# Kernel tuning notes

Hardware: AMD Instinct MI355X
Metric: run time of the kernel (lower is better)

Reference implementation:

```python
import jax, jax.numpy as jnp
import numpy as np

D_MODEL = 2048
NUM_HEADS = 16
KV_HEADS = 4
HEAD_DIM = D_MODEL // NUM_HEADS  # 128
SEQ = 4096
BATCH = 1
ROPE_THETA = 10000.0


def _rope_cache(T, dim, base, dtype):
    inv_freq = 1.0 / (base ** (jnp.arange(0, dim, 2, dtype=jnp.float32) / dim))
    t = jnp.arange(T, dtype=jnp.float32)
    freqs = jnp.outer(t, inv_freq)                      # (T, dim/2)
    emb = jnp.concatenate([freqs, freqs], axis=-1)      # (T, dim)
    return jnp.cos(emb).astype(dtype), jnp.sin(emb).astype(dtype)


def _rotate_half(x):
    d = x.shape[-1] // 2
    return jnp.concatenate([-x[..., d:], x[..., :d]], axis=-1)


def _apply_rope(q, k, cos, sin):
    # q: (B,T,Hq,D), k: (B,T,Hkv,D); cos/sin: (T,D) broadcast over heads
    c = cos[None, :, None, :]
    s = sin[None, :, None, :]
    q = q * c + _rotate_half(q) * s
    k = k * c + _rotate_half(k) * s
    return q, k


def setup_inputs() -> dict:
    key = jax.random.key(0)
    ks = jax.random.split(key, 6)
    sc = 1.0 / np.sqrt(D_MODEL)
    kv_out = KV_HEADS * HEAD_DIM
    return {
        "x": jax.random.normal(ks[0], (BATCH, SEQ, D_MODEL), dtype=jnp.float32),
        "Wq": jax.random.normal(ks[1], (D_MODEL, D_MODEL), dtype=jnp.float32) * sc,
        "Wk": jax.random.normal(ks[2], (D_MODEL, kv_out), dtype=jnp.float32) * sc,
        "Wv": jax.random.normal(ks[3], (D_MODEL, kv_out), dtype=jnp.float32) * sc,
        "Wo": jax.random.normal(ks[4], (D_MODEL, D_MODEL), dtype=jnp.float32) * sc,
        "bo": jax.random.normal(ks[5], (D_MODEL,), dtype=jnp.float32) * 0.01,
    }


def reference(x, Wq, Wk, Wv, Wo, bo):
    B, T, _ = x.shape
    q = (x @ Wq).reshape(B, T, NUM_HEADS, HEAD_DIM)
    k = (x @ Wk).reshape(B, T, KV_HEADS, HEAD_DIM)
    v = (x @ Wv).reshape(B, T, KV_HEADS, HEAD_DIM)

    cos, sin = _rope_cache(T, HEAD_DIM, ROPE_THETA, x.dtype)
    q, k = _apply_rope(q, k, cos, sin)

    reps = NUM_HEADS // KV_HEADS
    k = jnp.repeat(k, reps, axis=2)  # repeat_interleave on head dim
    v = jnp.repeat(v, reps, axis=2)

    # (B,H,T,D)
    q = q.transpose(0, 2, 1, 3)
    k = k.transpose(0, 2, 1, 3)
    v = v.transpose(0, 2, 1, 3)

    scores = jnp.einsum("bhqd,bhkd->bhqk", q, k)
    causal = jnp.triu(jnp.ones((T, T), dtype=bool), k=1)
    scores = jnp.where(causal[None, None], -jnp.inf, scores)
    attn = jax.nn.softmax(scores / jnp.sqrt(jnp.asarray(HEAD_DIM, x.dtype)), axis=-1)

    ctx = jnp.einsum("bhqk,bhkd->bhqd", attn, v)
    ctx = ctx.transpose(0, 2, 1, 3).reshape(B, T, D_MODEL)
    return ctx @ Wo + bo
```

## Files before the change

### kernel.cpp

```cpp
#include <hip/hip_runtime.h>
#include <cstdint>
#include <cstddef>

#define SEQ 4096
#define DM  2048
#define NH  16
#define KVH 4
#define HD  128
#define QSCALE (0.08838834764831845f * 1.4426950408889634f)

typedef short bf16_t;
typedef __attribute__((ext_vector_type(8))) short bf16x8;
typedef __attribute__((ext_vector_type(4))) float f32x4;
typedef __attribute__((ext_vector_type(4))) unsigned uint32x4;

__device__ __forceinline__ bf16_t f2b(float f) {
  unsigned u = __builtin_bit_cast(unsigned, f);
  u += 0x7fffu + ((u >> 16) & 1u);
  return (bf16_t)(u >> 16);
}
__device__ __forceinline__ float b2f(bf16_t s) {
  unsigned u = ((unsigned)(unsigned short)s) << 16;
  return __builtin_bit_cast(float, u);
}
__device__ __forceinline__ unsigned cvtpk(float lo, float hi) {
  unsigned r;
  asm("v_cvt_pk_bf16_f32 %0, %1, %2" : "=v"(r) : "v"(lo), "v"(hi));
  return r;
}

__device__ __forceinline__ void gload_lds16(const void* gsrc, void* ldst) {
  __builtin_amdgcn_global_load_lds(
      (__attribute__((address_space(1))) void*)gsrc,
      (__attribute__((address_space(3))) void*)ldst, 16, 0, 0);
}

__global__ void cast_x_bf16(const float* __restrict__ x, bf16_t* __restrict__ xb, int n4) {
  int i = blockIdx.x * 256 + threadIdx.x;
  if (i >= n4) return;
  float4 v = ((const float4*)x)[i];
  union { bf16_t h[4]; unsigned long long u; } o;
  o.h[0] = f2b(v.x); o.h[1] = f2b(v.y); o.h[2] = f2b(v.z); o.h[3] = f2b(v.w);
  ((unsigned long long*)xb)[i] = o.u;
}

__global__ void transpose_cast_w(const float* __restrict__ W, bf16_t* __restrict__ Wt,
                                 int K, int N) {
  __shared__ float tile[32][33];
  int k0 = blockIdx.y * 32, n0 = blockIdx.x * 32;
  int tx = threadIdx.x, ty = threadIdx.y;
#pragma unroll
  for (int dy = 0; dy < 32; dy += 8)
    tile[ty + dy][tx] = W[(size_t)(k0 + ty + dy) * N + n0 + tx];
  __syncthreads();
#pragma unroll
  for (int dy = 0; dy < 32; dy += 8)
    Wt[(size_t)(n0 + ty + dy) * K + k0 + tx] = f2b(tile[tx][ty + dy]);
}

__global__ void rope_tab(float* __restrict__ ct, float* __restrict__ st) {
  int i = blockIdx.x * 256 + threadIdx.x;
  if (i >= SEQ * 64) return;
  int t = i >> 6, j = i & 63;
  float invf = expf(-(float)j * (9.210340371976184f / 64.0f));
  float ang = (float)t * invf;
  ct[i] = cosf(ang);
  st[i] = sinf(ang);
}

__global__ void rope_apply(bf16_t* __restrict__ Qb, bf16_t* __restrict__ KVb,
                           const float* __restrict__ ct, const float* __restrict__ st) {
  int i = blockIdx.x * 256 + threadIdx.x;
  const int qtot = SEQ * NH * 64;
  const int tot = qtot + SEQ * KVH * 64;
  if (i >= tot) return;
  bf16_t* base; int t, j; float scl;
  if (i < qtot) {
    t = i >> 10; int rem = i & 1023; int hh = rem >> 6; j = rem & 63;
    base = Qb + (size_t)t * DM + hh * HD;
    scl = QSCALE;
  } else {
    int i2 = i - qtot;
    t = i2 >> 8; int rem = i2 & 255; int hh = rem >> 6; j = rem & 63;
    base = KVb + (size_t)t * 1024 + hh * HD;
    scl = 1.0f;
  }
  float c = ct[t * 64 + j], s = st[t * 64 + j];
  float x0 = b2f(base[j]);
  float x1 = b2f(base[j + 64]);
  base[j]      = f2b((x0 * c - x1 * s) * scl);
  base[j + 64] = f2b((x1 * c + x0 * s) * scl);
}

__global__ void transpose_v(const bf16_t* __restrict__ KVb, bf16_t* __restrict__ Vt) {
  __shared__ bf16_t tile[32][33];
  int t0 = blockIdx.y * 32, d0 = blockIdx.x * 32;
  int tx = threadIdx.x, ty = threadIdx.y;
#pragma unroll
  for (int dy = 0; dy < 32; dy += 8)
    tile[ty + dy][tx] = KVb[(size_t)(t0 + ty + dy) * 1024 + 512 + d0 + tx];
  __syncthreads();
  int tt = t0 + tx;
  int j = (tt & ~63) | (tt & 32) | ((tt & 12) << 1) | ((tt & 16) >> 2) | (tt & 3);
#pragma unroll
  for (int dy = 0; dy < 32; dy += 8)
    Vt[(size_t)(d0 + ty + dy) * SEQ + j] = tile[tx][ty + dy];
}

template <int BIAS>
__global__ __launch_bounds__(256, 2)
void gemm_bt(const bf16_t* __restrict__ A, const bf16_t* __restrict__ Bt,
             void* __restrict__ Cout, const float* __restrict__ bias,
             int M, int N, int K) {
  __shared__ __align__(16) bf16_t ldsA[128 * 64];
  __shared__ __align__(16) bf16_t ldsB[128 * 64];
  const int t = threadIdx.x;
  const int w = t >> 6, l = t & 63;
  const int lg = l >> 4, lr = l & 15;
  const int bm = blockIdx.y, bn = blockIdx.x;
  const int wr = (w >> 1) * 64, wc = (w & 1) * 64;

  f32x4 acc[4][4] = {};

  for (int k0 = 0; k0 < K; k0 += 64) {
    __syncthreads();
#pragma unroll
    for (int i = 0; i < 4; ++i) {
      int idx = i * 256 + t;
      int row = idx >> 3;
      int ch  = (idx & 7) ^ (row & 7);
      gload_lds16(A  + (size_t)(bm * 128 + row) * K + k0 + ch * 8, &ldsA[idx * 8]);
      gload_lds16(Bt + (size_t)(bn * 128 + row) * K + k0 + ch * 8, &ldsB[idx * 8]);
    }
    __syncthreads();
#pragma unroll
    for (int kk = 0; kk < 2; ++kk) {
      bf16x8 af[4], bfr[4];
#pragma unroll
      for (int m = 0; m < 4; ++m) {
        int row = wr + m * 16 + lr;
        int ch = (kk * 4 + lg) ^ (row & 7);
        af[m] = *(const bf16x8*)&ldsA[row * 64 + ch * 8];
      }
#pragma unroll
      for (int n = 0; n < 4; ++n) {
        int row = wc + n * 16 + lr;
        int ch = (kk * 4 + lg) ^ (row & 7);
        bfr[n] = *(const bf16x8*)&ldsB[row * 64 + ch * 8];
      }
#pragma unroll
      for (int m = 0; m < 4; ++m)
#pragma unroll
        for (int n = 0; n < 4; ++n)
          acc[m][n] = __builtin_amdgcn_mfma_f32_16x16x32_bf16(af[m], bfr[n], acc[m][n], 0, 0, 0);
    }
  }

  const int row0 = bm * 128 + wr + lg * 4;
  const int col0 = bn * 128 + wc + lr;
  if (BIAS) {
    float* C = (float*)Cout;
#pragma unroll
    for (int n = 0; n < 4; ++n) {
      int col = col0 + n * 16;
      float b = bias[col];
#pragma unroll
      for (int m = 0; m < 4; ++m)
#pragma unroll
        for (int r = 0; r < 4; ++r)
          C[(size_t)(row0 + m * 16 + r) * N + col] = acc[m][n][r] + b;
    }
  } else {
    bf16_t* C = (bf16_t*)Cout;
#pragma unroll
    for (int m = 0; m < 4; ++m)
#pragma unroll
      for (int n = 0; n < 4; ++n) {
        int col = col0 + n * 16;
#pragma unroll
        for (int r = 0; r < 4; ++r)
          C[(size_t)(row0 + m * 16 + r) * N + col] = f2b(acc[m][n][r]);
      }
  }
}

__global__ __launch_bounds__(256, 2)
void attn_fwd(const bf16_t* __restrict__ Qb, const bf16_t* __restrict__ KVb,
              const bf16_t* __restrict__ Vt, bf16_t* __restrict__ ctx) {
  __shared__ __align__(16) bf16_t kt[2][64 * 128];
  __shared__ __align__(16) bf16_t vts[2][128 * 64];

  const int t = threadIdx.x;
  const int w = t >> 6, l = t & 63;
  const int lg = l >> 4, lr = l & 15;
  const int h = blockIdx.y, g = h >> 2;
  const int b = blockIdx.x;
  const int qt0 = b, qt1 = 63 - b;

  bf16x8 qf[2][4];
#pragma unroll
  for (int kk = 0; kk < 4; ++kk) {
    qf[0][kk] = *(const bf16x8*)&Qb[(size_t)(qt0 * 64 + w * 16 + lr) * DM + h * HD + kk * 32 + lg * 8];
    qf[1][kk] = *(const bf16x8*)&Qb[(size_t)(qt1 * 64 + w * 16 + lr) * DM + h * HD + kk * 32 + lg * 8];
  }

  f32x4 acc[2][9] = {};
  float m_run[2] = {-1e30f, -1e30f};

  bf16x8 ones;
#pragma unroll
  for (int i = 0; i < 8; ++i) ones[i] = (short)0x3F80;

  const bf16_t* ksrc = KVb + g * 128;
  const bf16_t* vsrc = Vt + (size_t)(g * 128) * SEQ;
  auto stage = [&](int buf, int kvt) {
#pragma unroll
    for (int i = 0; i < 4; ++i) {
      int idx = i * 256 + t;
      int row = idx >> 4;
      int ch = (idx & 15) ^ (row & 7);
      gload_lds16(ksrc + (size_t)(kvt * 64 + row) * 1024 + ch * 8, &kt[buf][idx * 8]);
    }
#pragma unroll
    for (int i = 0; i < 4; ++i) {
      int idx = i * 256 + t;
      int row = idx >> 3;
      int ch = (idx & 7) ^ (row & 7);
      gload_lds16(vsrc + (size_t)row * SEQ + kvt * 64 + ch * 8, &vts[buf][idx * 8]);
    }
  };

  const int nkv = qt1 + 1;
  stage(0, 0);

  for (int kv = 0; kv < nkv; ++kv) {
    const int cur = kv & 1;
    const int kv0 = kv * 64;
    __syncthreads();
    if (kv + 1 < nkv) stage(cur ^ 1, kv + 1);

    const bool act0 = kv <= qt0;

    f32x4 s[2][4];
#pragma unroll
    for (int m = 0; m < 2; ++m)
#pragma unroll
      for (int n = 0; n < 4; ++n) s[m][n] = f32x4{0.f, 0.f, 0.f, 0.f};

    __builtin_amdgcn_s_setprio(1);
#pragma unroll
    for (int n = 0; n < 4; ++n) {
      int row = n * 16 + lr;
#pragma unroll
      for (int kk = 0; kk < 4; ++kk) {
        int ch = (kk * 4 + lg) ^ (row & 7);
        bf16x8 kf = *(const bf16x8*)&kt[cur][row * 128 + ch * 8];
        if (act0) s[0][n] = __builtin_amdgcn_mfma_f32_16x16x32_bf16(kf, qf[0][kk], s[0][n], 0, 0, 0);
        s[1][n] = __builtin_amdgcn_mfma_f32_16x16x32_bf16(kf, qf[1][kk], s[1][n], 0, 0, 0);
      }
    }
    __builtin_amdgcn_s_setprio(0);

    auto softmax = [&](f32x4 (&sv)[4], float& mr, f32x4 (&am)[9], int qtm,
                       bf16x8 (&pf)[2]) {
      const int qrow = qtm * 64 + w * 16 + lr;
      if (kv == qtm) {
#pragma unroll
        for (int n = 0; n < 4; ++n)
#pragma unroll
          for (int r = 0; r < 4; ++r) {
            int key = kv0 + n * 16 + lg * 4 + r;
            if (key > qrow) sv[n][r] = -1e30f;
          }
      }
      float pm = sv[0][0];
#pragma unroll
      for (int n = 0; n < 4; ++n)
#pragma unroll
        for (int r = 0; r < 4; ++r)
          pm = fmaxf(pm, sv[n][r]);
      pm = fmaxf(pm, __shfl_xor(pm, 16, 64));
      pm = fmaxf(pm, __shfl_xor(pm, 32, 64));

      if (__any((int)(pm > mr + 8.f))) {
        float mn = fmaxf(mr, pm);
        float a_s = exp2f(mr - mn);
        mr = mn;
        float alpha[4];
#pragma unroll
        for (int r = 0; r < 4; ++r)
          alpha[r] = __shfl(a_s, (l & 48) | (lg * 4 + r), 64);
#pragma unroll
        for (int nd = 0; nd < 9; ++nd)
#pragma unroll
          for (int r = 0; r < 4; ++r)
            am[nd][r] *= alpha[r];
      }

      unsigned u[8];
#pragma unroll
      for (int n = 0; n < 4; ++n) {
        u[2 * n]     = cvtpk(exp2f(sv[n][0] - mr), exp2f(sv[n][1] - mr));
        u[2 * n + 1] = cvtpk(exp2f(sv[n][2] - mr), exp2f(sv[n][3] - mr));
      }
      pf[0] = __builtin_bit_cast(bf16x8, (uint32x4){u[0], u[1], u[2], u[3]});
      pf[1] = __builtin_bit_cast(bf16x8, (uint32x4){u[4], u[5], u[6], u[7]});
    };

    auto loadvf = [&](bf16x8 (&vf)[8], int kk2) {
#pragma unroll
      for (int nd = 0; nd < 8; ++nd) {
        int vrow = nd * 16 + lr;
        int ch = (kk2 * 4 + lg) ^ (lr & 7);
        vf[nd] = *(const bf16x8*)&vts[cur][vrow * 64 + ch * 8];
      }
    };
    auto pv = [&](const bf16x8 (&vf)[8], const bf16x8& pfk, f32x4 (&am)[9]) {
      __builtin_amdgcn_s_setprio(1);
#pragma unroll
      for (int nd = 0; nd < 8; ++nd)
        am[nd] = __builtin_amdgcn_mfma_f32_16x16x32_bf16(pfk, vf[nd], am[nd], 0, 0, 0);
      am[8] = __builtin_amdgcn_mfma_f32_16x16x32_bf16(pfk, ones, am[8], 0, 0, 0);
      __builtin_amdgcn_s_setprio(0);
    };

    bf16x8 pf0[2], pf1[2];
    if (act0) softmax(s[0], m_run[0], acc[0], qt0, pf0);
    bf16x8 vfa[8];
    loadvf(vfa, 0);
    if (act0) pv(vfa, pf0[0], acc[0]);
    softmax(s[1], m_run[1], acc[1], qt1, pf1);
    pv(vfa, pf1[0], acc[1]);
    bf16x8 vfb[8];
    loadvf(vfb, 1);
    if (act0) pv(vfb, pf0[1], acc[0]);
    pv(vfb, pf1[1], acc[1]);
  }

#pragma unroll
  for (int m = 0; m < 2; ++m) {
    const int qtm = (m == 0) ? qt0 : qt1;
#pragma unroll
    for (int r = 0; r < 4; ++r) {
      float rl = 1.0f / acc[m][8][r];
      int qrow = qtm * 64 + w * 16 + lg * 4 + r;
#pragma unroll
      for (int nd = 0; nd < 8; ++nd) {
        int col = h * HD + nd * 16 + lr;
        ctx[(size_t)qrow * DM + col] = f2b(acc[m][nd][r] * rl);
      }
    }
  }
}

extern "C" void kernel_launch(void* const* d_in, const int* in_sizes, int n_in,
                              void* d_out, int out_size, void* d_ws, size_t ws_size,
                              hipStream_t stream) {
  const float* x  = (const float*)d_in[0];
  const float* Wq = (const float*)d_in[1];
  const float* Wk = (const float*)d_in[2];
  const float* Wv = (const float*)d_in[3];
  const float* Wo = (const float*)d_in[4];
  const float* bo = (const float*)d_in[5];
  float* out = (float*)d_out;

  char* p = (char*)d_ws;
  bf16_t* xb   = (bf16_t*)p;
  bf16_t* ctx  = xb;
  p += (size_t)SEQ * DM * 2;
  bf16_t* Wqt  = (bf16_t*)p; p += (size_t)DM * DM * 2;
  bf16_t* Wkvt = (bf16_t*)p; p += (size_t)1024 * DM * 2;
  bf16_t* Wot  = (bf16_t*)p; p += (size_t)DM * DM * 2;
  bf16_t* Qb   = (bf16_t*)p; p += (size_t)SEQ * DM * 2;
  bf16_t* KVb  = (bf16_t*)p; p += (size_t)SEQ * 1024 * 2;
  bf16_t* Vt   = (bf16_t*)p; p += (size_t)512 * SEQ * 2;
  float*  ctab = (float*)p;  p += (size_t)SEQ * 64 * 4;
  float*  stab = (float*)p;  p += (size_t)SEQ * 64 * 4;

  cast_x_bf16<<<(SEQ * DM / 4 + 255) / 256, 256, 0, stream>>>(x, xb, SEQ * DM / 4);
  transpose_cast_w<<<dim3(DM / 32, DM / 32), dim3(32, 8), 0, stream>>>(Wq, Wqt, DM, DM);
  transpose_cast_w<<<dim3(512 / 32, DM / 32), dim3(32, 8), 0, stream>>>(Wk, Wkvt, DM, 512);
  transpose_cast_w<<<dim3(512 / 32, DM / 32), dim3(32, 8), 0, stream>>>(Wv, Wkvt + (size_t)512 * DM, DM, 512);
  transpose_cast_w<<<dim3(DM / 32, DM / 32), dim3(32, 8), 0, stream>>>(Wo, Wot, DM, DM);
  rope_tab<<<(SEQ * 64 + 255) / 256, 256, 0, stream>>>(ctab, stab);

  gemm_bt<0><<<dim3(DM / 128, SEQ / 128), 256, 0, stream>>>(xb, Wqt, Qb, nullptr, SEQ, DM, DM);
  gemm_bt<0><<<dim3(1024 / 128, SEQ / 128), 256, 0, stream>>>(xb, Wkvt, KVb, nullptr, SEQ, 1024, DM);

  rope_apply<<<(SEQ * (NH + KVH) * 64 + 255) / 256, 256, 0, stream>>>(Qb, KVb, ctab, stab);
  transpose_v<<<dim3(512 / 32, SEQ / 32), dim3(32, 8), 0, stream>>>(KVb, Vt);

  attn_fwd<<<dim3(32, NH), 256, 0, stream>>>(Qb, KVb, Vt, ctx);

  gemm_bt<1><<<dim3(DM / 128, SEQ / 128), 256, 0, stream>>>(ctx, Wot, out, bo, SEQ, DM, DM);
}
```

Measured before the change: 281.3 us.

## Split paired query tiles across two wave groups in 512-thread attention blocks

The attention kernel now launches 512 threads per block. Waves 0-3 handle the early query tile and waves 4-7 handle the mirrored late tile, instead of each wave processing both tiles. The K/V staging loads are spread across twice as many threads, and each wave keeps a single accumulator set. This cuts per-thread register pressure and raises the wave count, at the cost of load imbalance: the short-tile waves sit idle at barriers while the long-tile waves continue through later KV blocks.

```diff
diff --git a/kernel.cpp b/kernel.cpp
--- a/kernel.cpp
+++ b/kernel.cpp
@@ -184,7 +184,7 @@
   }
 }
 
-__global__ __launch_bounds__(256, 2)
+__global__ __launch_bounds__(512, 4)
 void attn_fwd(const bf16_t* __restrict__ Qb, const bf16_t* __restrict__ KVb,
               const bf16_t* __restrict__ Vt, bf16_t* __restrict__ ctx) {
   __shared__ __align__(16) bf16_t kt[2][64 * 128];
@@ -195,17 +195,17 @@
   const int lg = l >> 4, lr = l & 15;
   const int h = blockIdx.y, g = h >> 2;
   const int b = blockIdx.x;
-  const int qt0 = b, qt1 = 63 - b;
-
-  bf16x8 qf[2][4];
-#pragma unroll
-  for (int kk = 0; kk < 4; ++kk) {
-    qf[0][kk] = *(const bf16x8*)&Qb[(size_t)(qt0 * 64 + w * 16 + lr) * DM + h * HD + kk * 32 + lg * 8];
-    qf[1][kk] = *(const bf16x8*)&Qb[(size_t)(qt1 * 64 + w * 16 + lr) * DM + h * HD + kk * 32 + lg * 8];
-  }
-
-  f32x4 acc[2][9] = {};
-  float m_run[2] = {-1e30f, -1e30f};
+  const int m = w >> 2, wq = w & 3;
+  const int qt = m ? 63 - b : b;
+  const int qrow0 = qt * 64 + wq * 16;
+
+  bf16x8 qf[4];
+#pragma unroll
+  for (int kk = 0; kk < 4; ++kk)
+    qf[kk] = *(const bf16x8*)&Qb[(size_t)(qrow0 + lr) * DM + h * HD + kk * 32 + lg * 8];
+
+  f32x4 acc[9] = {};
+  float m_run = -1e30f;
 
   bf16x8 ones;
 #pragma unroll
@@ -215,22 +215,22 @@
   const bf16_t* vsrc = Vt + (size_t)(g * 128) * SEQ;
   auto stage = [&](int buf, int kvt) {
 #pragma unroll
-    for (int i = 0; i < 4; ++i) {
-      int idx = i * 256 + t;
+    for (int i = 0; i < 2; ++i) {
+      int idx = i * 512 + t;
       int row = idx >> 4;
       int ch = (idx & 15) ^ (row & 7);
       gload_lds16(ksrc + (size_t)(kvt * 64 + row) * 1024 + ch * 8, &kt[buf][idx * 8]);
     }
 #pragma unroll
-    for (int i = 0; i < 4; ++i) {
-      int idx = i * 256 + t;
+    for (int i = 0; i < 2; ++i) {
+      int idx = i * 512 + t;
       int row = idx >> 3;
       int ch = (idx & 7) ^ (row & 7);
       gload_lds16(vsrc + (size_t)row * SEQ + kvt * 64 + ch * 8, &vts[buf][idx * 8]);
     }
   };
 
-  const int nkv = qt1 + 1;
+  const int nkv = 64 - b;
   stage(0, 0);
 
   for (int kv = 0; kv < nkv; ++kv) {
@@ -239,53 +239,45 @@
     __syncthreads();
     if (kv + 1 < nkv) stage(cur ^ 1, kv + 1);
 
-    const bool act0 = kv <= qt0;
-
-    f32x4 s[2][4];
-#pragma unroll
-    for (int m = 0; m < 2; ++m)
-#pragma unroll
-      for (int n = 0; n < 4; ++n) s[m][n] = f32x4{0.f, 0.f, 0.f, 0.f};
-
-    __builtin_amdgcn_s_setprio(1);
-#pragma unroll
-    for (int n = 0; n < 4; ++n) {
-      int row = n * 16 + lr;
-#pragma unroll
-      for (int kk = 0; kk < 4; ++kk) {
-        int ch = (kk * 4 + lg) ^ (row & 7);
-        bf16x8 kf = *(const bf16x8*)&kt[cur][row * 128 + ch * 8];
-        if (act0) s[0][n] = __builtin_amdgcn_mfma_f32_16x16x32_bf16(kf, qf[0][kk], s[0][n], 0, 0, 0);
-        s[1][n] = __builtin_amdgcn_mfma_f32_16x16x32_bf16(kf, qf[1][kk], s[1][n], 0, 0, 0);
-      }
-    }
-    __builtin_amdgcn_s_setprio(0);
-
-    auto softmax = [&](f32x4 (&sv)[4], float& mr, f32x4 (&am)[9], int qtm,
-                       bf16x8 (&pf)[2]) {
-      const int qrow = qtm * 64 + w * 16 + lr;
-      if (kv == qtm) {
+    if (kv <= qt) {
+      f32x4 s[4] = {};
+      __builtin_amdgcn_s_setprio(1);
+#pragma unroll
+      for (int n = 0; n < 4; ++n) {
+        int row = n * 16 + lr;
+#pragma unroll
+        for (int kk = 0; kk < 4; ++kk) {
+          int ch = (kk * 4 + lg) ^ (row & 7);
+          bf16x8 kf = *(const bf16x8*)&kt[cur][row * 128 + ch * 8];
+          s[n] = __builtin_amdgcn_mfma_f32_16x16x32_bf16(kf, qf[kk], s[n], 0, 0, 0);
+        }
+      }
+      __builtin_amdgcn_s_setprio(0);
+
+      const int qrow = qrow0 + lr;
+      if (kv == qt) {
 #pragma unroll
         for (int n = 0; n < 4; ++n)
 #pragma unroll
           for (int r = 0; r < 4; ++r) {
             int key = kv0 + n * 16 + lg * 4 + r;
-            if (key > qrow) sv[n][r] = -1e30f;
+            if (key > qrow) s[n][r] = -1e30f;
           }
       }
-      float pm = sv[0][0];
+
+      float pm = s[0][0];
 #pragma unroll
       for (int n = 0; n < 4; ++n)
 #pragma unroll
         for (int r = 0; r < 4; ++r)
-          pm = fmaxf(pm, sv[n][r]);
+          pm = fmaxf(pm, s[n][r]);
       pm = fmaxf(pm, __shfl_xor(pm, 16, 64));
       pm = fmaxf(pm, __shfl_xor(pm, 32, 64));
 
-      if (__any((int)(pm > mr + 8.f))) {
-        float mn = fmaxf(mr, pm);
-        float a_s = exp2f(mr - mn);
-        mr = mn;
+      if (__any((int)(pm > m_run + 8.f))) {
+        float mn = fmaxf(m_run, pm);
+        float a_s = exp2f(m_run - mn);
+        m_run = mn;
         float alpha[4];
 #pragma unroll
         for (int r = 0; r < 4; ++r)
@@ -294,61 +286,43 @@
         for (int nd = 0; nd < 9; ++nd)
 #pragma unroll
           for (int r = 0; r < 4; ++r)
-            am[nd][r] *= alpha[r];
+            acc[nd][r] *= alpha[r];
       }
 
       unsigned u[8];
 #pragma unroll
       for (int n = 0; n < 4; ++n) {
-        u[2 * n]     = cvtpk(exp2f(sv[n][0] - mr), exp2f(sv[n][1] - mr));
-        u[2 * n + 1] = cvtpk(exp2f(sv[n][2] - mr), exp2f(sv[n][3] - mr));
-      }
+        u[2 * n]     = cvtpk(exp2f(s[n][0] - m_run), exp2f(s[n][1] - m_run));
+        u[2 * n + 1] = cvtpk(exp2f(s[n][2] - m_run), exp2f(s[n][3] - m_run));
+      }
+      bf16x8 pf[2];
       pf[0] = __builtin_bit_cast(bf16x8, (uint32x4){u[0], u[1], u[2], u[3]});
       pf[1] = __builtin_bit_cast(bf16x8, (uint32x4){u[4], u[5], u[6], u[7]});
-    };
-
-    auto loadvf = [&](bf16x8 (&vf)[8], int kk2) {
-#pragma unroll
-      for (int nd = 0; nd < 8; ++nd) {
-        int vrow = nd * 16 + lr;
-        int ch = (kk2 * 4 + lg) ^ (lr & 7);
-        vf[nd] = *(const bf16x8*)&vts[cur][vrow * 64 + ch * 8];
-      }
-    };
-    auto pv = [&](const bf16x8 (&vf)[8], const bf16x8& pfk, f32x4 (&am)[9]) {
+
       __builtin_amdgcn_s_setprio(1);
 #pragma unroll
-      for (int nd = 0; nd < 8; ++nd)
-        am[nd] = __builtin_amdgcn_mfma_f32_16x16x32_bf16(pfk, vf[nd], am[nd], 0, 0, 0);
-      am[8] = __builtin_amdgcn_mfma_f32_16x16x32_bf16(pfk, ones, am[8], 0, 0, 0);
+      for (int kk2 = 0; kk2 < 2; ++kk2) {
+#pragma unroll
+        for (int nd = 0; nd < 8; ++nd) {
+          int vrow = nd * 16 + lr;
+          int vch = (kk2 * 4 + lg) ^ (lr & 7);
+          bf16x8 vf = *(const bf16x8*)&vts[cur][vrow * 64 + vch * 8];
+          acc[nd] = __builtin_amdgcn_mfma_f32_16x16x32_bf16(pf[kk2], vf, acc[nd], 0, 0, 0);
+        }
+        acc[8] = __builtin_amdgcn_mfma_f32_16x16x32_bf16(pf[kk2], ones, acc[8], 0, 0, 0);
+      }
       __builtin_amdgcn_s_setprio(0);
-    };
-
-    bf16x8 pf0[2], pf1[2];
-    if (act0) softmax(s[0], m_run[0], acc[0], qt0, pf0);
-    bf16x8 vfa[8];
-    loadvf(vfa, 0);
-    if (act0) pv(vfa, pf0[0], acc[0]);
-    softmax(s[1], m_run[1], acc[1], qt1, pf1);
-    pv(vfa, pf1[0], acc[1]);
-    bf16x8 vfb[8];
-    loadvf(vfb, 1);
-    if (act0) pv(vfb, pf0[1], acc[0]);
-    pv(vfb, pf1[1], acc[1]);
-  }
-
-#pragma unroll
-  for (int m = 0; m < 2; ++m) {
-    const int qtm = (m == 0) ? qt0 : qt1;
-#pragma unroll
-    for (int r = 0; r < 4; ++r) {
-      float rl = 1.0f / acc[m][8][r];
-      int qrow = qtm * 64 + w * 16 + lg * 4 + r;
-#pragma unroll
-      for (int nd = 0; nd < 8; ++nd) {
-        int col = h * HD + nd * 16 + lr;
-        ctx[(size_t)qrow * DM + col] = f2b(acc[m][nd][r] * rl);
-      }
+    }
+  }
+
+#pragma unroll
+  for (int r = 0; r < 4; ++r) {
+    float rl = 1.0f / acc[8][r];
+    int qrow = qrow0 + lg * 4 + r;
+#pragma unroll
+    for (int nd = 0; nd < 8; ++nd) {
+      int col = h * HD + nd * 16 + lr;
+      ctx[(size_t)qrow * DM + col] = f2b(acc[nd][r] * rl);
     }
   }
 }
@@ -390,7 +364,7 @@
   rope_apply<<<(SEQ * (NH + KVH) * 64 + 255) / 256, 256, 0, stream>>>(Qb, KVb, ctab, stab);
   transpose_v<<<dim3(512 / 32, SEQ / 32), dim3(32, 8), 0, stream>>>(KVb, Vt);
 
-  attn_fwd<<<dim3(32, NH), 256, 0, stream>>>(Qb, KVb, Vt, ctx);
+  attn_fwd<<<dim3(32, NH), 512, 0, stream>>>(Qb, KVb, Vt, ctx);
 
   gemm_bt<1><<<dim3(DM / 128, SEQ / 128), 256, 0, stream>>>(ctx, Wot, out, bo, SEQ, DM, DM);
 }
```

Result: faster. 275.4 us (-2.1%).
